# Kernel optimization log

Measured on AMD Instinct MI355X. Metric: run time of the kernel, lower is better.

The kernel has to match this reference:

```python
import jax, jax.numpy as jnp
import numpy as np

N, L = 64, 128
D = (32, 16, 8)   # input mode dims
H = (32, 16, 8)   # hidden mode dims


def setup_inputs() -> dict:
    key = jax.random.key(0)
    ks = jax.random.split(key, 7)
    inputs = jax.random.normal(ks[0], (N, L, *D), dtype=jnp.float32)
    # 3 gates (z, r, h) stacked along leading axis g; one factor matrix per mode.
    W1 = jax.random.normal(ks[1], (3, H[0], D[0]), dtype=jnp.float32) * 0.1
    W2 = jax.random.normal(ks[2], (3, H[1], D[1]), dtype=jnp.float32) * 0.1
    W3 = jax.random.normal(ks[3], (3, H[2], D[2]), dtype=jnp.float32) * 0.1
    U1 = jax.random.normal(ks[4], (3, H[0], H[0]), dtype=jnp.float32) * 0.1
    U2 = jax.random.normal(ks[5], (3, H[1], H[1]), dtype=jnp.float32) * 0.1
    U3 = jax.random.normal(ks[6], (3, H[2], H[2]), dtype=jnp.float32) * 0.1
    return {"inputs": inputs, "W1": W1, "W2": W2, "W3": W3,
            "U1": U1, "U2": U2, "U3": U3}


def reference(inputs, W1, W2, W3, U1, U2, U3):
    # batch_first -> (L, N, a, b, c)
    x = jnp.transpose(inputs, (1, 0, 2, 3, 4))
    # Precompute input projections for all timesteps and all 3 gates at once
    # (same math as applying TCL per step; mode-wise tensor contraction).
    XW = jnp.einsum('lnabc,gda,geb,gfc->lgndef', x, W1, W2, W3)  # (L,3,N,h1,h2,h3)
    h0 = jnp.zeros((x.shape[1], U1.shape[1], U2.shape[1], U3.shape[1]), x.dtype)

    def step(h, xw):
        hu = jnp.einsum('nabc,gda,geb,gfc->gndef', h, U1, U2, U3)  # (3,N,h1,h2,h3)
        z = jax.nn.sigmoid(xw[0] + hu[0])
        r = jax.nn.sigmoid(xw[1] + hu[1])
        hh = jnp.tanh(xw[2] + r * hu[2])
        h_new = z * h + (1.0 - z) * hh
        return h_new, h_new

    h_last, outs = jax.lax.scan(step, h0, XW)          # outs: (L,N,h1,h2,h3)
    outs = jnp.transpose(outs, (1, 0, 2, 3, 4))         # back to batch_first
    return outs, h_last
```

## Files before the change

### kernel.cpp

```cpp
#include <hip/hip_runtime.h>
#include <stdint.h>


constexpr int kN = 64;
constexpr int kL = 128;
constexpr int kA = 32, kB = 16, kC = 8;
constexpr int kBC = kB * kC;
constexpr int kTot = kA * kBC;
constexpr int kTS = kBC + 4;
constexpr int kTh = 512;
constexpr int kXwTiles = 16;

constexpr int kHTS = 40;
constexpr int kT1S = 136;

typedef __attribute__((ext_vector_type(8))) short bf16x8;
typedef __attribute__((ext_vector_type(4))) float f32x4;

namespace {

__device__ __forceinline__ float bf2f(unsigned int u) { return __uint_as_float(u << 16); }
__device__ __forceinline__ unsigned int f2bf(float v) {
  unsigned int u = __float_as_uint(v);
  return (u + 0x7fffu + ((u >> 16) & 1u)) >> 16;
}
__device__ __forceinline__ float sigmoid_f(float x) {
  return __fdividef(1.f, 1.f + __expf(-x));
}
__device__ __forceinline__ float tanh_f(float x) {
  return 1.f - __fdividef(2.f, 1.f + __expf(2.f * x));
}

__device__ __forceinline__ bf16x8 frag_from_lds(const unsigned short* p) {
  uint4 u = *(const uint4*)p;
  return __builtin_bit_cast(bf16x8, u);
}
__device__ __forceinline__ bf16x8 frag_from_f32(const float* p) {
  float4 a = ((const float4*)p)[0];
  float4 b = ((const float4*)p)[1];
  uint4 u;
  u.x = f2bf(a.x) | (f2bf(a.y) << 16);
  u.y = f2bf(a.z) | (f2bf(a.w) << 16);
  u.z = f2bf(b.x) | (f2bf(b.y) << 16);
  u.w = f2bf(b.z) | (f2bf(b.w) << 16);
  return __builtin_bit_cast(bf16x8, u);
}
__device__ __forceinline__ uint2 pack4(const f32x4& a) {
  uint2 p;
  p.x = f2bf(a[0]) | (f2bf(a[1]) << 16);
  p.y = f2bf(a[2]) | (f2bf(a[3]) << 16);
  return p;
}
__device__ __forceinline__ uint4 pack8(const float* v) {
  uint4 u;
  u.x = f2bf(v[0]) | (f2bf(v[1]) << 16);
  u.y = f2bf(v[2]) | (f2bf(v[3]) << 16);
  u.z = f2bf(v[4]) | (f2bf(v[5]) << 16);
  u.w = f2bf(v[6]) | (f2bf(v[7]) << 16);
  return u;
}

__global__ void kron_kernel(const float* __restrict__ W2, const float* __restrict__ W3,
                            const float* __restrict__ U2, const float* __restrict__ U3,
                            unsigned short* __restrict__ kW, unsigned short* __restrict__ kU) {
  int i = blockIdx.x * 256 + threadIdx.x;
  const float* M2 = W2; const float* M3 = W3; unsigned short* dst = kW;
  int j = i;
  if (i >= 3 * 128 * 128) { M2 = U2; M3 = U3; dst = kU; j = i - 3 * 128 * 128; }
  int g = j >> 14, ef = (j >> 7) & 127, bc = j & 127;
  int e = ef >> 3, f = ef & 7, b = bc >> 3, c = bc & 7;
  float v = M2[(g * 16 + e) * 16 + b] * M3[(g * 8 + f) * 8 + c];
  dst[j] = (unsigned short)f2bf(v);
}

__device__ __forceinline__ void gemm1(const unsigned short* __restrict__ srcT,
                                      const bf16x8 bW[3][2],
                                      unsigned short (*__restrict__ t1L)[kA * kT1S],
                                      int w, int q, int r) {
  bf16x8 ah = frag_from_lds(srcT + (w * 16 + r) * kHTS + q * 8);
#pragma unroll
  for (int g = 0; g < 3; ++g) {
#pragma unroll
    for (int nt = 0; nt < 2; ++nt) {
      f32x4 acc = {0.f, 0.f, 0.f, 0.f};
      acc = __builtin_amdgcn_mfma_f32_16x16x32_bf16(ah, bW[g][nt], acc, 0, 0, 0);
      *(uint2*)&t1L[g][(nt * 16 + r) * kT1S + w * 16 + q * 4] = pack4(acc);
    }
  }
}

__device__ __forceinline__ void gemm2_scan(const unsigned short (*__restrict__ t1L)[kA * kT1S],
                                           const bf16x8 bK[3][2][4],
                                           f32x4 out2[3][2],
                                           int mtw, int q, int r) {
  const int abase = (mtw * 16 + r) * kT1S + q * 8;
#pragma unroll
  for (int g = 0; g < 3; ++g) {
    bf16x8 af[4];
#pragma unroll
    for (int kc = 0; kc < 4; ++kc)
      af[kc] = frag_from_lds(&t1L[g][abase + kc * 32]);
#pragma unroll
    for (int eft = 0; eft < 2; ++eft) {
      f32x4 acc = {0.f, 0.f, 0.f, 0.f};
#pragma unroll
      for (int kc = 0; kc < 4; ++kc)
        acc = __builtin_amdgcn_mfma_f32_16x16x32_bf16(af[kc], bK[g][eft][kc], acc, 0, 0, 0);
      out2[g][eft] = acc;
    }
  }
}

__device__ __forceinline__ void load_bfrags_scan(const unsigned short* __restrict__ kron,
                                                 const float* __restrict__ M1,
                                                 bf16x8 bK[3][2][4], bf16x8 bW[3][2],
                                                 int efb, int q, int r) {
#pragma unroll
  for (int g = 0; g < 3; ++g) {
#pragma unroll
    for (int eft = 0; eft < 2; ++eft)
#pragma unroll
      for (int kc = 0; kc < 4; ++kc)
        bK[g][eft][kc] = frag_from_lds(
            kron + ((g * 128 + (efb + 4 * eft) * 16 + r) * 128 + kc * 32 + q * 8));
#pragma unroll
    for (int nt = 0; nt < 2; ++nt)
      bW[g][nt] = frag_from_f32(M1 + (g * 32 + nt * 16 + r) * 32 + q * 8);
  }
}

__global__ __launch_bounds__(kTh) void xw_mfma(
    const float* __restrict__ x, const float* __restrict__ W1,
    const unsigned short* __restrict__ kW, unsigned short* __restrict__ xw) {
  __shared__ __align__(16) unsigned short xT[2][kBC * kHTS];
  __shared__ __align__(16) unsigned short t1L[3][kA * kT1S];
  const int tid = threadIdx.x;
  const int w = tid >> 6, l = tid & 63, q = l >> 4, r = l & 15;

  bf16x8 bK[3][4], bW[3][2];
#pragma unroll
  for (int g = 0; g < 3; ++g) {
#pragma unroll
    for (int kc = 0; kc < 4; ++kc)
      bK[g][kc] = frag_from_lds(kW + ((g * 128 + w * 16 + r) * 128 + kc * 32 + q * 8));
#pragma unroll
    for (int nt = 0; nt < 2; ++nt)
      bW[g][nt] = frag_from_f32(W1 + (g * 32 + nt * 16 + r) * 32 + q * 8);
  }

  const int bc = tid & 127, a0 = (tid >> 7) * 8;
  const int eftOfs = (w >> 2) * 4;
  const int blk0 = blockIdx.x * kXwTiles;

  float xr[8];
  {
    const float* xg = x + (size_t)blk0 * kTot + bc;
#pragma unroll
    for (int j = 0; j < 8; ++j) xr[j] = xg[(a0 + j) * kBC];
    *(uint4*)&xT[0][bc * kHTS + a0] = pack8(xr);
  }
  __syncthreads();

  for (int tt = 0; tt < kXwTiles; ++tt) {
    const int blk = blk0 + tt;
    {
      const int nx = (tt + 1 < kXwTiles) ? tt + 1 : tt;
      const float* xg = x + (size_t)(blk0 + nx) * kTot + bc;
#pragma unroll
      for (int j = 0; j < 8; ++j) xr[j] = xg[(a0 + j) * kBC];
    }
    gemm1(xT[tt & 1], bW, t1L, w, q, r);
    __syncthreads();
    f32x4 out2[3][2];
#pragma unroll
    for (int g = 0; g < 3; ++g) {
#pragma unroll
      for (int mt = 0; mt < 2; ++mt) {
        f32x4 acc = {0.f, 0.f, 0.f, 0.f};
#pragma unroll
        for (int kc = 0; kc < 4; ++kc) {
          bf16x8 af = frag_from_lds(&t1L[g][(mt * 16 + r) * kT1S + kc * 32 + q * 8]);
          acc = __builtin_amdgcn_mfma_f32_16x16x32_bf16(af, bK[g][kc], acc, 0, 0, 0);
        }
        out2[g][mt] = acc;
      }
    }
#pragma unroll
    for (int g = 0; g < 3; ++g) {
      unsigned short* xo = xw + ((size_t)blk * 3 + g) * kTot;
#pragma unroll
      for (int mt = 0; mt < 2; ++mt) {
        const int wp = ((w & 3) << 1) | mt;
        uint2 p = pack4(out2[g][mt]);
        *(uint2*)(xo + (wp * 64 + q * 16 + r) * 8 + eftOfs) = p;
      }
    }
    *(uint4*)&xT[(tt + 1) & 1][bc * kHTS + a0] = pack8(xr);
    __syncthreads();
  }
}

__global__ __launch_bounds__(kTh) void scan_mfma(
    const unsigned short* __restrict__ xw, const float* __restrict__ U1,
    const unsigned short* __restrict__ kU,
    float* __restrict__ outs, float* __restrict__ hlast) {
  __shared__ __align__(16) unsigned short hT[kBC * kHTS];
  __shared__ __align__(16) unsigned short t1L[3][kA * kT1S];
  const int tid = threadIdx.x;
  const int n = blockIdx.x;
  const int w = tid >> 6, l = tid & 63, q = l >> 4, r = l & 15;
  const int mtw = w & 1, efb = w >> 1;
  const int dbase = mtw * 16 + q * 4;

  bf16x8 bK[3][2][4], bW[3][2];
  load_bfrags_scan(kU, U1, bK, bW, efb, q, r);

  for (int i = tid; i < kBC * kHTS / 2; i += kTh) ((unsigned int*)hT)[i] = 0u;
  float hreg[2][4] = {{0.f, 0.f, 0.f, 0.f}, {0.f, 0.f, 0.f, 0.f}};

  const unsigned short* xp = xw + (size_t)n * kL * 3 * kTot + tid * 8;
  unsigned int xc[3][4];
#pragma unroll
  for (int g = 0; g < 3; ++g) {
    uint4 u = *(const uint4*)(xp + g * kTot);
    xc[g][0] = u.x; xc[g][1] = u.y; xc[g][2] = u.z; xc[g][3] = u.w;
  }
  __syncthreads();

  for (int t = 0; t < kL; ++t) {
    unsigned int xn[3][4];
    {
      const unsigned short* xq = xp + (size_t)((t + 1 < kL) ? t + 1 : t) * 3 * kTot;
#pragma unroll
      for (int g = 0; g < 3; ++g) {
        uint4 u = *(const uint4*)(xq + g * kTot);
        xn[g][0] = u.x; xn[g][1] = u.y; xn[g][2] = u.z; xn[g][3] = u.w;
      }
    }
    gemm1(hT, bW, t1L, w, q, r);
    __syncthreads();
    f32x4 hu[3][2];
    gemm2_scan(t1L, bK, hu, mtw, q, r);

    const size_t obase = ((size_t)n * kL + t) * kTot;
#pragma unroll
    for (int eft = 0; eft < 2; ++eft) {
      const int ef = (efb + 4 * eft) * 16 + r;
#pragma unroll
      for (int i = 0; i < 4; ++i) {
        const int e2 = eft * 4 + i;
        float x0 = bf2f((e2 & 1) ? (xc[0][e2 >> 1] >> 16) : (xc[0][e2 >> 1] & 0xffffu));
        float x1 = bf2f((e2 & 1) ? (xc[1][e2 >> 1] >> 16) : (xc[1][e2 >> 1] & 0xffffu));
        float x2 = bf2f((e2 & 1) ? (xc[2][e2 >> 1] >> 16) : (xc[2][e2 >> 1] & 0xffffu));
        float z  = sigmoid_f(x0 + hu[0][eft][i]);
        float rr = sigmoid_f(x1 + hu[1][eft][i]);
        float hc = tanh_f(x2 + rr * hu[2][eft][i]);
        float hn = z * hreg[eft][i] + (1.f - z) * hc;
        hreg[eft][i] = hn;
        outs[obase + (size_t)(dbase + i) * kBC + ef] = hn;
      }
      uint2 p;
      p.x = f2bf(hreg[eft][0]) | (f2bf(hreg[eft][1]) << 16);
      p.y = f2bf(hreg[eft][2]) | (f2bf(hreg[eft][3]) << 16);
      *(uint2*)&hT[ef * kHTS + dbase] = p;
    }
#pragma unroll
    for (int g = 0; g < 3; ++g)
#pragma unroll
      for (int u = 0; u < 4; ++u) xc[g][u] = xn[g][u];
    __syncthreads();
  }
#pragma unroll
  for (int eft = 0; eft < 2; ++eft) {
    const int ef = (efb + 4 * eft) * 16 + r;
#pragma unroll
    for (int i = 0; i < 4; ++i)
      hlast[(size_t)n * kTot + (size_t)(dbase + i) * kBC + ef] = hreg[eft][i];
  }
}

__device__ __forceinline__ int rfl(int v) { return __builtin_amdgcn_readfirstlane(v); }

__device__ __forceinline__ void load8f(const float* p, float* v) {
  float4 a = ((const float4*)p)[0];
  float4 b = ((const float4*)p)[1];
  v[0]=a.x; v[1]=a.y; v[2]=a.z; v[3]=a.w;
  v[4]=b.x; v[5]=b.y; v[6]=b.z; v[7]=b.w;
}
__device__ __forceinline__ void store8f(float* p, const float* v) {
  ((float4*)p)[0] = make_float4(v[0],v[1],v[2],v[3]);
  ((float4*)p)[1] = make_float4(v[4],v[5],v[6],v[7]);
}

__device__ __forceinline__ void mode1(const float* __restrict__ src,
                                      const float* __restrict__ Wg,
                                      float* __restrict__ t1, int tid) {
  const int w = rfl(tid >> 6);
  const int lane = tid & 63;
  const int bc = ((w & 1) << 6) | lane;
  const int dq = (w >> 1) << 3;
  float xr[kA];
#pragma unroll
  for (int a = 0; a < kA; ++a) xr[a] = src[a * kBC + bc];
  const float* wp = Wg + dq * kA;
#pragma unroll
  for (int dd = 0; dd < 8; ++dd) {
    float s = 0.f;
#pragma unroll
    for (int a = 0; a < kA; ++a) s += wp[dd * kA + a] * xr[a];
    t1[(dq + dd) * kTS + bc] = s;
  }
}
__device__ __forceinline__ void mode2(const float* __restrict__ t1,
                                      const float* __restrict__ Wg,
                                      float* __restrict__ t2, int tid) {
  const int w = rfl(tid >> 6);
  const int lane = tid & 63;
  const int d = ((w >> 1) << 3) | (lane >> 3);
  const int c = lane & 7;
  const int eh = (w & 1) << 3;
  float tr[kB];
#pragma unroll
  for (int b = 0; b < kB; ++b) tr[b] = t1[d * kTS + b * kC + c];
#pragma unroll
  for (int ee = 0; ee < 8; ++ee) {
    const int e = eh + ee;
    float s = 0.f;
#pragma unroll
    for (int b = 0; b < kB; ++b) s += Wg[e * kB + b] * tr[b];
    t2[d * kTS + e * kC + c] = s;
  }
}
__device__ __forceinline__ void mode3(const float* __restrict__ t2,
                                      const float* __restrict__ Wg,
                                      float* __restrict__ out8, int tid) {
  const int e = tid & 15;
  const int d = tid >> 4;
  float tr[kC];
  load8f(t2 + d * kTS + e * kC, tr);
#pragma unroll
  for (int f = 0; f < kC; ++f) {
    float s = 0.f;
#pragma unroll
    for (int c = 0; c < kC; ++c) s += Wg[f * kC + c] * tr[c];
    out8[f] = s;
  }
}

__global__ __launch_bounds__(kTh) void fused_kernel(
    const float* __restrict__ x,
    const float* __restrict__ W1, const float* __restrict__ W2,
    const float* __restrict__ W3, const float* __restrict__ U1,
    const float* __restrict__ U2, const float* __restrict__ U3,
    float* __restrict__ outs, float* __restrict__ hlast) {
  __shared__ float h[kTot];
  __shared__ float xs[kTot];
  __shared__ float t1[kA * kTS];
  __shared__ float t2[kA * kTS];
  const int tid = threadIdx.x;
  const int n = blockIdx.x;
  for (int i = tid; i < kTot; i += kTh) h[i] = 0.f;
  const int off = tid * kC;
  float* hp = h + off;
  float hn[kC];
  for (int l = 0; l < kL; ++l) {
    const float4* xg = (const float4*)(x + ((size_t)n * kL + l) * kTot);
    float4 xa = xg[tid], xb = xg[tid + kTh];
    __syncthreads();
    float4* xs4 = (float4*)xs;
    xs4[tid] = xa;
    xs4[tid + kTh] = xb;
    __syncthreads();
    float xwv[3][kC], hu[3][kC];
#pragma unroll
    for (int g = 0; g < 3; ++g) {
      mode1(xs, W1 + g * kA * kA, t1, tid);
      __syncthreads();
      mode2(t1, W2 + g * kB * kB, t2, tid);
      __syncthreads();
      mode3(t2, W3 + g * kC * kC, xwv[g], tid);
    }
#pragma unroll
    for (int g = 0; g < 3; ++g) {
      mode1(h, U1 + g * kA * kA, t1, tid);
      __syncthreads();
      mode2(t1, U2 + g * kB * kB, t2, tid);
      __syncthreads();
      mode3(t2, U3 + g * kC * kC, hu[g], tid);
    }
    float ho[kC];
    load8f(hp, ho);
#pragma unroll
    for (int f = 0; f < kC; ++f) {
      float z  = sigmoid_f(xwv[0][f] + hu[0][f]);
      float rr = sigmoid_f(xwv[1][f] + hu[1][f]);
      float hh = tanh_f(xwv[2][f] + rr * hu[2][f]);
      hn[f] = z * ho[f] + (1.f - z) * hh;
    }
    store8f(hp, hn);
    store8f(outs + ((size_t)n * kL + l) * kTot + off, hn);
  }
  store8f(hlast + (size_t)n * kTot + off, hn);
}

}

extern "C" void kernel_launch(void* const* d_in, const int* in_sizes, int n_in,
                              void* d_out, int out_size, void* d_ws, size_t ws_size,
                              hipStream_t stream) {
  const float* x  = (const float*)d_in[0];
  const float* W1 = (const float*)d_in[1];
  const float* W2 = (const float*)d_in[2];
  const float* W3 = (const float*)d_in[3];
  const float* U1 = (const float*)d_in[4];
  const float* U2 = (const float*)d_in[5];
  const float* U3 = (const float*)d_in[6];
  float* outs  = (float*)d_out;
  float* hlast = outs + (size_t)kN * kL * kTot;

  const size_t kron_elems = 3 * 128 * 128;
  const size_t kron_bytes = 2 * kron_elems * sizeof(unsigned short);
  const size_t xw_bytes   = (size_t)kN * kL * 3 * kTot * 2;

  if (ws_size >= kron_bytes + xw_bytes) {
    unsigned short* kW  = (unsigned short*)d_ws;
    unsigned short* kU  = kW + kron_elems;
    unsigned short* xww = kU + kron_elems;
    kron_kernel<<<dim3(384), dim3(256), 0, stream>>>(W2, W3, U2, U3, kW, kU);
    xw_mfma<<<dim3(kN * kL / kXwTiles), dim3(kTh), 0, stream>>>(x, W1, kW, xww);
    scan_mfma<<<dim3(kN), dim3(kTh), 0, stream>>>(xww, U1, kU, outs, hlast);
  } else {
    fused_kernel<<<dim3(kN), dim3(kTh), 0, stream>>>(x, W1, W2, W3, U1, U2, U3,
                                                     outs, hlast);
  }
}
```

Measured before the change: 588.0 us.

## Fuse input projection and scan into one persistent kernel with flag handoff

Replaces the separate xw projection kernel and scan kernel with a single launch of 64 scan blocks plus 448 producer blocks. Producers compute XW tiles in timestep-major order and publish per-tile readiness flags with a threadfence and atomic store. Scan blocks spin on those flags two steps ahead, so the projection overlaps the latency-bound recurrence instead of running before it. This relies on all 512 blocks being co-resident to avoid deadlock and adds polling and fence overhead.

Result: slower. 1.223 ms (+108.0%).

```diff
diff --git a/kernel.cpp b/kernel.cpp
--- a/kernel.cpp
+++ b/kernel.cpp
@@ -9,10 +9,17 @@
 constexpr int kTot = kA * kBC;
 constexpr int kTS = kBC + 4;
 constexpr int kTh = 512;
-constexpr int kXwTiles = 16;
+
+constexpr int kScan = 64;
+constexpr int kProd = 448;
+constexpr int kTiles = kN * kL;
 
 constexpr int kHTS = 40;
 constexpr int kT1S = 136;
+
+constexpr int kXTBytes = kBC * kHTS * 2;
+constexpr int kT1Bytes = 3 * kA * kT1S * 2;
+constexpr int kSmemBytes = 2 * kXTBytes + kT1Bytes;
 
 typedef __attribute__((ext_vector_type(8))) short bf16x8;
 typedef __attribute__((ext_vector_type(4))) float f32x4;
@@ -62,8 +69,10 @@
 
 __global__ void kron_kernel(const float* __restrict__ W2, const float* __restrict__ W3,
                             const float* __restrict__ U2, const float* __restrict__ U3,
-                            unsigned short* __restrict__ kW, unsigned short* __restrict__ kU) {
+                            unsigned short* __restrict__ kW, unsigned short* __restrict__ kU,
+                            unsigned int* __restrict__ flags) {
   int i = blockIdx.x * 256 + threadIdx.x;
+  if (i < kTiles) flags[i] = 0u;
   const float* M2 = W2; const float* M3 = W3; unsigned short* dst = kW;
   int j = i;
   if (i >= 3 * 128 * 128) { M2 = U2; M3 = U3; dst = kU; j = i - 3 * 128 * 128; }
@@ -89,193 +98,203 @@
   }
 }
 
-__device__ __forceinline__ void gemm2_scan(const unsigned short (*__restrict__ t1L)[kA * kT1S],
-                                           const bf16x8 bK[3][2][4],
-                                           f32x4 out2[3][2],
-                                           int mtw, int q, int r) {
-  const int abase = (mtw * 16 + r) * kT1S + q * 8;
-#pragma unroll
-  for (int g = 0; g < 3; ++g) {
-    bf16x8 af[4];
-#pragma unroll
-    for (int kc = 0; kc < 4; ++kc)
-      af[kc] = frag_from_lds(&t1L[g][abase + kc * 32]);
-#pragma unroll
-    for (int eft = 0; eft < 2; ++eft) {
-      f32x4 acc = {0.f, 0.f, 0.f, 0.f};
-#pragma unroll
-      for (int kc = 0; kc < 4; ++kc)
-        acc = __builtin_amdgcn_mfma_f32_16x16x32_bf16(af[kc], bK[g][eft][kc], acc, 0, 0, 0);
-      out2[g][eft] = acc;
-    }
-  }
-}
-
-__device__ __forceinline__ void load_bfrags_scan(const unsigned short* __restrict__ kron,
-                                                 const float* __restrict__ M1,
-                                                 bf16x8 bK[3][2][4], bf16x8 bW[3][2],
-                                                 int efb, int q, int r) {
-#pragma unroll
-  for (int g = 0; g < 3; ++g) {
-#pragma unroll
-    for (int eft = 0; eft < 2; ++eft)
-#pragma unroll
-      for (int kc = 0; kc < 4; ++kc)
-        bK[g][eft][kc] = frag_from_lds(
-            kron + ((g * 128 + (efb + 4 * eft) * 16 + r) * 128 + kc * 32 + q * 8));
-#pragma unroll
-    for (int nt = 0; nt < 2; ++nt)
-      bW[g][nt] = frag_from_f32(M1 + (g * 32 + nt * 16 + r) * 32 + q * 8);
-  }
-}
-
-__global__ __launch_bounds__(kTh) void xw_mfma(
+__global__ __launch_bounds__(kTh) void combo_kernel(
     const float* __restrict__ x, const float* __restrict__ W1,
-    const unsigned short* __restrict__ kW, unsigned short* __restrict__ xw) {
-  __shared__ __align__(16) unsigned short xT[2][kBC * kHTS];
-  __shared__ __align__(16) unsigned short t1L[3][kA * kT1S];
+    const float* __restrict__ U1, const unsigned short* __restrict__ kW,
+    const unsigned short* __restrict__ kU, unsigned short* __restrict__ xw,
+    unsigned int* __restrict__ flags,
+    float* __restrict__ outs, float* __restrict__ hlast) {
+  __shared__ __align__(16) unsigned char smem[kSmemBytes];
   const int tid = threadIdx.x;
   const int w = tid >> 6, l = tid & 63, q = l >> 4, r = l & 15;
 
-  bf16x8 bK[3][4], bW[3][2];
-#pragma unroll
-  for (int g = 0; g < 3; ++g) {
-#pragma unroll
-    for (int kc = 0; kc < 4; ++kc)
-      bK[g][kc] = frag_from_lds(kW + ((g * 128 + w * 16 + r) * 128 + kc * 32 + q * 8));
-#pragma unroll
-    for (int nt = 0; nt < 2; ++nt)
-      bW[g][nt] = frag_from_f32(W1 + (g * 32 + nt * 16 + r) * 32 + q * 8);
-  }
-
-  const int bc = tid & 127, a0 = (tid >> 7) * 8;
-  const int eftOfs = (w >> 2) * 4;
-  const int blk0 = blockIdx.x * kXwTiles;
-
-  float xr[8];
-  {
-    const float* xg = x + (size_t)blk0 * kTot + bc;
-#pragma unroll
-    for (int j = 0; j < 8; ++j) xr[j] = xg[(a0 + j) * kBC];
-    *(uint4*)&xT[0][bc * kHTS + a0] = pack8(xr);
-  }
-  __syncthreads();
-
-  for (int tt = 0; tt < kXwTiles; ++tt) {
-    const int blk = blk0 + tt;
+  if (blockIdx.x >= kScan) {
+    unsigned short (*xT)[kBC * kHTS] = (unsigned short(*)[kBC * kHTS])smem;
+    unsigned short (*t1L)[kA * kT1S] =
+        (unsigned short(*)[kA * kT1S])(smem + 2 * kXTBytes);
+    const int p = blockIdx.x - kScan;
+
+    bf16x8 bK[3][4], bW[3][2];
+#pragma unroll
+    for (int g = 0; g < 3; ++g) {
+#pragma unroll
+      for (int kc = 0; kc < 4; ++kc)
+        bK[g][kc] = frag_from_lds(kW + ((g * 128 + w * 16 + r) * 128 + kc * 32 + q * 8));
+#pragma unroll
+      for (int nt = 0; nt < 2; ++nt)
+        bW[g][nt] = frag_from_f32(W1 + (g * 32 + nt * 16 + r) * 32 + q * 8);
+    }
+
+    const int bc = tid & 127, a0 = (tid >> 7) * 8;
+    const int eftOfs = (w >> 2) * 4;
+
+    float xr[8];
     {
-      const int nx = (tt + 1 < kXwTiles) ? tt + 1 : tt;
-      const float* xg = x + (size_t)(blk0 + nx) * kTot + bc;
+      const int t0 = p >> 6, n0 = p & 63;
+      const float* xg = x + (size_t)(n0 * kL + t0) * kTot + bc;
 #pragma unroll
       for (int j = 0; j < 8; ++j) xr[j] = xg[(a0 + j) * kBC];
-    }
-    gemm1(xT[tt & 1], bW, t1L, w, q, r);
+      *(uint4*)&xT[0][bc * kHTS + a0] = pack8(xr);
+    }
     __syncthreads();
-    f32x4 out2[3][2];
+    int buf = 0;
+    for (int idx = p; idx < kTiles; idx += kProd) {
+      {
+        const int nx = (idx + kProd < kTiles) ? idx + kProd : idx;
+        const int tn = nx >> 6, nn2 = nx & 63;
+        const float* xg = x + (size_t)(nn2 * kL + tn) * kTot + bc;
+#pragma unroll
+        for (int j = 0; j < 8; ++j) xr[j] = xg[(a0 + j) * kBC];
+      }
+      gemm1(xT[buf], bW, t1L, w, q, r);
+      __syncthreads();
+      f32x4 out2[3][2];
+#pragma unroll
+      for (int g = 0; g < 3; ++g) {
+#pragma unroll
+        for (int mt = 0; mt < 2; ++mt) {
+          f32x4 acc = {0.f, 0.f, 0.f, 0.f};
+#pragma unroll
+          for (int kc = 0; kc < 4; ++kc) {
+            bf16x8 af = frag_from_lds(&t1L[g][(mt * 16 + r) * kT1S + kc * 32 + q * 8]);
+            acc = __builtin_amdgcn_mfma_f32_16x16x32_bf16(af, bK[g][kc], acc, 0, 0, 0);
+          }
+          out2[g][mt] = acc;
+        }
+      }
+      const int tt = idx >> 6, nn = idx & 63;
+      const size_t blk = (size_t)nn * kL + tt;
+#pragma unroll
+      for (int g = 0; g < 3; ++g) {
+        unsigned short* xo = xw + (blk * 3 + g) * kTot;
+#pragma unroll
+        for (int mt = 0; mt < 2; ++mt) {
+          const int wp = ((w & 3) << 1) | mt;
+          uint2 pv = pack4(out2[g][mt]);
+          *(uint2*)(xo + (wp * 64 + q * 16 + r) * 8 + eftOfs) = pv;
+        }
+      }
+      *(uint4*)&xT[buf ^ 1][bc * kHTS + a0] = pack8(xr);
+      __syncthreads();
+      if (tid == 0) {
+        __threadfence();
+        atomicExch(&flags[blk], 1u);
+      }
+      buf ^= 1;
+    }
+  } else {
+    unsigned short* hT = (unsigned short*)smem;
+    unsigned short (*t1L)[kA * kT1S] =
+        (unsigned short(*)[kA * kT1S])(smem + kXTBytes);
+    const int n = blockIdx.x;
+    const int mtw = w & 1, efb = w >> 1;
+    const int dbase = mtw * 16 + q * 4;
+    unsigned int* fl = flags + n * kL;
+
+    bf16x8 bKU[3][2][4], bWu[3][2];
 #pragma unroll
     for (int g = 0; g < 3; ++g) {
 #pragma unroll
-      for (int mt = 0; mt < 2; ++mt) {
-        f32x4 acc = {0.f, 0.f, 0.f, 0.f};
-#pragma unroll
-        for (int kc = 0; kc < 4; ++kc) {
-          bf16x8 af = frag_from_lds(&t1L[g][(mt * 16 + r) * kT1S + kc * 32 + q * 8]);
-          acc = __builtin_amdgcn_mfma_f32_16x16x32_bf16(af, bK[g][kc], acc, 0, 0, 0);
+      for (int eft = 0; eft < 2; ++eft)
+#pragma unroll
+        for (int kc = 0; kc < 4; ++kc)
+          bKU[g][eft][kc] = frag_from_lds(
+              kU + ((g * 128 + (efb + 4 * eft) * 16 + r) * 128 + kc * 32 + q * 8));
+#pragma unroll
+      for (int nt = 0; nt < 2; ++nt)
+        bWu[g][nt] = frag_from_f32(U1 + (g * 32 + nt * 16 + r) * 32 + q * 8);
+    }
+
+    for (int i = tid; i < kBC * kHTS / 2; i += kTh) ((unsigned int*)hT)[i] = 0u;
+    float hreg[2][4] = {{0.f, 0.f, 0.f, 0.f}, {0.f, 0.f, 0.f, 0.f}};
+
+    if (tid == 0) {
+      while (atomicAdd(&fl[0], 0u) == 0u) __builtin_amdgcn_s_sleep(8);
+      while (atomicAdd(&fl[1], 0u) == 0u) __builtin_amdgcn_s_sleep(8);
+      __threadfence();
+    }
+    __syncthreads();
+
+    const unsigned short* xp = xw + (size_t)n * kL * 3 * kTot + tid * 8;
+    unsigned int xc[3][4];
+#pragma unroll
+    for (int g = 0; g < 3; ++g) {
+      uint4 u = *(const uint4*)(xp + g * kTot);
+      xc[g][0] = u.x; xc[g][1] = u.y; xc[g][2] = u.z; xc[g][3] = u.w;
+    }
+
+    for (int t = 0; t < kL; ++t) {
+      unsigned int xn[3][4];
+      {
+        const unsigned short* xq = xp + (size_t)((t + 1 < kL) ? t + 1 : t) * 3 * kTot;
+#pragma unroll
+        for (int g = 0; g < 3; ++g) {
+          uint4 u = *(const uint4*)(xq + g * kTot);
+          xn[g][0] = u.x; xn[g][1] = u.y; xn[g][2] = u.z; xn[g][3] = u.w;
         }
-        out2[g][mt] = acc;
-      }
-    }
-#pragma unroll
-    for (int g = 0; g < 3; ++g) {
-      unsigned short* xo = xw + ((size_t)blk * 3 + g) * kTot;
-#pragma unroll
-      for (int mt = 0; mt < 2; ++mt) {
-        const int wp = ((w & 3) << 1) | mt;
-        uint2 p = pack4(out2[g][mt]);
-        *(uint2*)(xo + (wp * 64 + q * 16 + r) * 8 + eftOfs) = p;
-      }
-    }
-    *(uint4*)&xT[(tt + 1) & 1][bc * kHTS + a0] = pack8(xr);
-    __syncthreads();
-  }
-}
-
-__global__ __launch_bounds__(kTh) void scan_mfma(
-    const unsigned short* __restrict__ xw, const float* __restrict__ U1,
-    const unsigned short* __restrict__ kU,
-    float* __restrict__ outs, float* __restrict__ hlast) {
-  __shared__ __align__(16) unsigned short hT[kBC * kHTS];
-  __shared__ __align__(16) unsigned short t1L[3][kA * kT1S];
-  const int tid = threadIdx.x;
-  const int n = blockIdx.x;
-  const int w = tid >> 6, l = tid & 63, q = l >> 4, r = l & 15;
-  const int mtw = w & 1, efb = w >> 1;
-  const int dbase = mtw * 16 + q * 4;
-
-  bf16x8 bK[3][2][4], bW[3][2];
-  load_bfrags_scan(kU, U1, bK, bW, efb, q, r);
-
-  for (int i = tid; i < kBC * kHTS / 2; i += kTh) ((unsigned int*)hT)[i] = 0u;
-  float hreg[2][4] = {{0.f, 0.f, 0.f, 0.f}, {0.f, 0.f, 0.f, 0.f}};
-
-  const unsigned short* xp = xw + (size_t)n * kL * 3 * kTot + tid * 8;
-  unsigned int xc[3][4];
-#pragma unroll
-  for (int g = 0; g < 3; ++g) {
-    uint4 u = *(const uint4*)(xp + g * kTot);
-    xc[g][0] = u.x; xc[g][1] = u.y; xc[g][2] = u.z; xc[g][3] = u.w;
-  }
-  __syncthreads();
-
-  for (int t = 0; t < kL; ++t) {
-    unsigned int xn[3][4];
-    {
-      const unsigned short* xq = xp + (size_t)((t + 1 < kL) ? t + 1 : t) * 3 * kTot;
-#pragma unroll
-      for (int g = 0; g < 3; ++g) {
-        uint4 u = *(const uint4*)(xq + g * kTot);
-        xn[g][0] = u.x; xn[g][1] = u.y; xn[g][2] = u.z; xn[g][3] = u.w;
-      }
-    }
-    gemm1(hT, bW, t1L, w, q, r);
-    __syncthreads();
-    f32x4 hu[3][2];
-    gemm2_scan(t1L, bK, hu, mtw, q, r);
-
-    const size_t obase = ((size_t)n * kL + t) * kTot;
+      }
+      gemm1(hT, bWu, t1L, w, q, r);
+      __syncthreads();
+      f32x4 hu[3][2];
+      {
+        const int abase = (mtw * 16 + r) * kT1S + q * 8;
+#pragma unroll
+        for (int g = 0; g < 3; ++g) {
+          bf16x8 af[4];
+#pragma unroll
+          for (int kc = 0; kc < 4; ++kc)
+            af[kc] = frag_from_lds(&t1L[g][abase + kc * 32]);
+#pragma unroll
+          for (int eft = 0; eft < 2; ++eft) {
+            f32x4 acc = {0.f, 0.f, 0.f, 0.f};
+#pragma unroll
+            for (int kc = 0; kc < 4; ++kc)
+              acc = __builtin_amdgcn_mfma_f32_16x16x32_bf16(af[kc], bKU[g][eft][kc], acc,
+                                                            0, 0, 0);
+            hu[g][eft] = acc;
+          }
+        }
+      }
+
+      const size_t obase = ((size_t)n * kL + t) * kTot;
+#pragma unroll
+      for (int eft = 0; eft < 2; ++eft) {
+        const int ef = (efb + 4 * eft) * 16 + r;
+#pragma unroll
+        for (int i = 0; i < 4; ++i) {
+          const int e2 = eft * 4 + i;
+          float x0 = bf2f((e2 & 1) ? (xc[0][e2 >> 1] >> 16) : (xc[0][e2 >> 1] & 0xffffu));
+          float x1 = bf2f((e2 & 1) ? (xc[1][e2 >> 1] >> 16) : (xc[1][e2 >> 1] & 0xffffu));
+          float x2 = bf2f((e2 & 1) ? (xc[2][e2 >> 1] >> 16) : (xc[2][e2 >> 1] & 0xffffu));
+          float z  = sigmoid_f(x0 + hu[0][eft][i]);
+          float rr = sigmoid_f(x1 + hu[1][eft][i]);
+          float hc = tanh_f(x2 + rr * hu[2][eft][i]);
+          float hn = z * hreg[eft][i] + (1.f - z) * hc;
+          hreg[eft][i] = hn;
+          outs[obase + (size_t)(dbase + i) * kBC + ef] = hn;
+        }
+        uint2 pv;
+        pv.x = f2bf(hreg[eft][0]) | (f2bf(hreg[eft][1]) << 16);
+        pv.y = f2bf(hreg[eft][2]) | (f2bf(hreg[eft][3]) << 16);
+        *(uint2*)&hT[ef * kHTS + dbase] = pv;
+      }
+#pragma unroll
+      for (int g = 0; g < 3; ++g)
+#pragma unroll
+        for (int u = 0; u < 4; ++u) xc[g][u] = xn[g][u];
+      if (tid == 0 && t + 2 < kL) {
+        while (atomicAdd(&fl[t + 2], 0u) == 0u) __builtin_amdgcn_s_sleep(8);
+        __threadfence();
+      }
+      __syncthreads();
+    }
 #pragma unroll
     for (int eft = 0; eft < 2; ++eft) {
       const int ef = (efb + 4 * eft) * 16 + r;
 #pragma unroll
-      for (int i = 0; i < 4; ++i) {
-        const int e2 = eft * 4 + i;
-        float x0 = bf2f((e2 & 1) ? (xc[0][e2 >> 1] >> 16) : (xc[0][e2 >> 1] & 0xffffu));
-        float x1 = bf2f((e2 & 1) ? (xc[1][e2 >> 1] >> 16) : (xc[1][e2 >> 1] & 0xffffu));
-        float x2 = bf2f((e2 & 1) ? (xc[2][e2 >> 1] >> 16) : (xc[2][e2 >> 1] & 0xffffu));
-        float z  = sigmoid_f(x0 + hu[0][eft][i]);
-        float rr = sigmoid_f(x1 + hu[1][eft][i]);
-        float hc = tanh_f(x2 + rr * hu[2][eft][i]);
-        float hn = z * hreg[eft][i] + (1.f - z) * hc;
-        hreg[eft][i] = hn;
-        outs[obase + (size_t)(dbase + i) * kBC + ef] = hn;
-      }
-      uint2 p;
-      p.x = f2bf(hreg[eft][0]) | (f2bf(hreg[eft][1]) << 16);
-      p.y = f2bf(hreg[eft][2]) | (f2bf(hreg[eft][3]) << 16);
-      *(uint2*)&hT[ef * kHTS + dbase] = p;
-    }
-#pragma unroll
-    for (int g = 0; g < 3; ++g)
-#pragma unroll
-      for (int u = 0; u < 4; ++u) xc[g][u] = xn[g][u];
-    __syncthreads();
-  }
-#pragma unroll
-  for (int eft = 0; eft < 2; ++eft) {
-    const int ef = (efb + 4 * eft) * 16 + r;
-#pragma unroll
-    for (int i = 0; i < 4; ++i)
-      hlast[(size_t)n * kTot + (size_t)(dbase + i) * kBC + ef] = hreg[eft][i];
+      for (int i = 0; i < 4; ++i)
+        hlast[(size_t)n * kTot + (size_t)(dbase + i) * kBC + ef] = hreg[eft][i];
+    }
   }
 }
 
@@ -420,15 +439,17 @@
 
   const size_t kron_elems = 3 * 128 * 128;
   const size_t kron_bytes = 2 * kron_elems * sizeof(unsigned short);
+  const size_t flag_bytes = (size_t)kTiles * sizeof(unsigned int);
   const size_t xw_bytes   = (size_t)kN * kL * 3 * kTot * 2;
 
-  if (ws_size >= kron_bytes + xw_bytes) {
-    unsigned short* kW  = (unsigned short*)d_ws;
-    unsigned short* kU  = kW + kron_elems;
-    unsigned short* xww = kU + kron_elems;
-    kron_kernel<<<dim3(384), dim3(256), 0, stream>>>(W2, W3, U2, U3, kW, kU);
-    xw_mfma<<<dim3(kN * kL / kXwTiles), dim3(kTh), 0, stream>>>(x, W1, kW, xww);
-    scan_mfma<<<dim3(kN), dim3(kTh), 0, stream>>>(xww, U1, kU, outs, hlast);
+  if (ws_size >= kron_bytes + flag_bytes + xw_bytes) {
+    unsigned short* kW = (unsigned short*)d_ws;
+    unsigned short* kU = kW + kron_elems;
+    unsigned int* flags = (unsigned int*)(kU + kron_elems);
+    unsigned short* xww = (unsigned short*)(flags + kTiles);
+    kron_kernel<<<dim3(384), dim3(256), 0, stream>>>(W2, W3, U2, U3, kW, kU, flags);
+    combo_kernel<<<dim3(kScan + kProd), dim3(kTh), 0, stream>>>(
+        x, W1, U1, kW, kU, xww, flags, outs, hlast);
   } else {
     fused_kernel<<<dim3(kN), dim3(kTh), 0, stream>>>(x, W1, W2, W3, U1, U2, U3,
                                                      outs, hlast);
```
